# Performance work log

Measured on AMD Instinct MI355X. Metric: run time of the kernel, lower is better.

Reference implementation:

```python
import jax, jax.numpy as jnp
import numpy as np

C = 256        # channels
HEADS = 4
D = C // HEADS # per-head dim
M = 3          # num modalities
EPS = 1e-5
NEG_SLOPE = 0.2  # PyG GATv2 leaky_relu slope


def setup_inputs() -> dict:
    key = jax.random.key(0)
    ks = iter(jax.random.split(key, 40))
    def nrm(shape, s=0.02):
        return jax.random.normal(next(ks), shape, dtype=jnp.float32) * s
    B, H, W = 2, 128, 128
    inp = {}
    for m in range(M):
        inp[f"modal{m}"] = jax.random.normal(next(ks), (B, C, H, W), dtype=jnp.float32)
    # fusion node initializer MLP: Linear-ReLU-Linear
    inp["fn_w1"] = nrm((C, C)); inp["fn_b1"] = jnp.zeros((C,), jnp.float32)
    inp["fn_w2"] = nrm((C, C)); inp["fn_b2"] = jnp.zeros((C,), jnp.float32)
    # two GATv2 layers + layernorms
    for l in range(2):
        inp[f"l{l}_wl"] = nrm((C, C)); inp[f"l{l}_bl"] = jnp.zeros((C,), jnp.float32)
        inp[f"l{l}_wr"] = nrm((C, C)); inp[f"l{l}_br"] = jnp.zeros((C,), jnp.float32)
        inp[f"l{l}_att"] = nrm((HEADS, D), 0.1)
        inp[f"l{l}_bias"] = jnp.zeros((C,), jnp.float32)
        inp[f"ln{l}_g"] = jnp.ones((C,), jnp.float32)
        inp[f"ln{l}_b"] = jnp.zeros((C,), jnp.float32)
    # spatial interaction: conv3x3 (no bias) + BN (eval mode) + ReLU
    inp["conv_w"] = nrm((C, C, 3, 3))
    inp["bn_g"] = jnp.ones((C,), jnp.float32); inp["bn_b"] = jnp.zeros((C,), jnp.float32)
    inp["bn_m"] = jnp.zeros((C,), jnp.float32); inp["bn_v"] = jnp.ones((C,), jnp.float32)
    return inp


def _gatv2(x, wl, bl, wr, br, att, bias):
    # Dense batched GATv2 over P tiny complete graphs (self-loops included,
    # matching PyG GATv2Conv add_self_loops=True default).
    P, N, Cc = x.shape
    xl = (x @ wl + bl).reshape(P, N, HEADS, D)  # source / message features
    xr = (x @ wr + br).reshape(P, N, HEADS, D)  # target features
    e = jax.nn.leaky_relu(xr[:, :, None] + xl[:, None, :], NEG_SLOPE)  # [P,Ni,Nj,H,D]
    scores = jnp.einsum('pijhd,hd->pijh', e, att)
    alpha = jax.nn.softmax(scores, axis=2)  # softmax over source nodes j per target i
    out = jnp.einsum('pijh,pjhd->pihd', alpha, xl)
    return out.reshape(P, N, Cc) + bias


def _layernorm(x, g, b):
    mu = jnp.mean(x, axis=-1, keepdims=True)
    var = jnp.mean((x - mu) ** 2, axis=-1, keepdims=True)
    return (x - mu) * jax.lax.rsqrt(var + EPS) * g + b


def _forward(modal0, modal1, modal2, fn_w1, fn_b1, fn_w2, fn_b2,
             l0_wl, l0_bl, l0_wr, l0_br, l0_att, l0_bias, ln0_g, ln0_b,
             l1_wl, l1_bl, l1_wr, l1_br, l1_att, l1_bias, ln1_g, ln1_b,
             conv_w, bn_g, bn_b, bn_m, bn_v):
    B, _, H, W = modal0.shape
    stacked = jnp.stack([modal0, modal1, modal2], axis=1)        # [B,M,C,H,W]
    modal_nodes = stacked.transpose(0, 3, 4, 1, 2).reshape(-1, M, C)  # [P,M,C]
    mean_feat = jnp.mean(modal_nodes, axis=1, keepdims=True)     # [P,1,C]
    fusion = jax.nn.relu(mean_feat @ fn_w1 + fn_b1) @ fn_w2 + fn_b2
    x = jnp.concatenate([fusion, modal_nodes], axis=1)           # [P,M+1,C]
    for (wl, bl, wr, br, att, bias, g, b) in (
        (l0_wl, l0_bl, l0_wr, l0_br, l0_att, l0_bias, ln0_g, ln0_b),
        (l1_wl, l1_bl, l1_wr, l1_br, l1_att, l1_bias, ln1_g, ln1_b),
    ):
        x = _layernorm(_gatv2(x, wl, bl, wr, br, att, bias) + x, g, b)
    fused = x[:, 0, :].reshape(B, H, W, C).transpose(0, 3, 1, 2)  # [B,C,H,W]
    y = jax.lax.conv_general_dilated(
        fused, conv_w, window_strides=(1, 1), padding='SAME',
        dimension_numbers=('NCHW', 'OIHW', 'NCHW'))
    bc = lambda v: v[None, :, None, None]
    y = (y - bc(bn_m)) * bc(jax.lax.rsqrt(bn_v + EPS)) * bc(bn_g) + bc(bn_b)
    y = jax.nn.relu(y)
    return y + fused


def reference(modal0, modal1, modal2, fn_w1, fn_b1, fn_w2, fn_b2,
              l0_wl, l0_bl, l0_wr, l0_br, l0_att, l0_bias, ln0_g, ln0_b,
              l1_wl, l1_bl, l1_wr, l1_br, l1_att, l1_bias, ln1_g, ln1_b,
              conv_w, bn_g, bn_b, bn_m, bn_v):
    return _forward(modal0, modal1, modal2, fn_w1, fn_b1, fn_w2, fn_b2,
                    l0_wl, l0_bl, l0_wr, l0_br, l0_att, l0_bias, ln0_g, ln0_b,
                    l1_wl, l1_bl, l1_wr, l1_br, l1_att, l1_bias, ln1_g, ln1_b,
                    conv_w, bn_g, bn_b, bn_m, bn_v)
```

## Files before the change

kernel.cpp:

```cpp
#include <hip/hip_runtime.h>


#define Pn 32768
#define PADR 16900

typedef __attribute__((ext_vector_type(8))) short bf16x8;
typedef __attribute__((ext_vector_type(4))) float f32x4;
typedef __attribute__((ext_vector_type(4))) unsigned short u16x4;
typedef __attribute__((ext_vector_type(8))) unsigned short u16x8;
typedef __attribute__((ext_vector_type(2))) unsigned int u32x2;

__device__ __forceinline__ float b2f(short s) {
  unsigned u = ((unsigned)(unsigned short)s) << 16;
  float f;
  __builtin_memcpy(&f, &u, 4);
  return f;
}
__device__ __forceinline__ float asf(unsigned u) {
  float f;
  __builtin_memcpy(&f, &u, 4);
  return f;
}
__device__ __forceinline__ short f2b(float f) {
  unsigned u;
  __builtin_memcpy(&u, &f, 4);
  u += 0x7fffu + ((u >> 16) & 1u);
  return (short)(u >> 16);
}
__device__ __forceinline__ float ldany(const void* p, int i, int bf) {
  return bf ? b2f(((const short*)p)[i]) : ((const float*)p)[i];
}
__device__ __forceinline__ void gload_lds16(const short* g, short* l) {
  __builtin_amdgcn_global_load_lds(
      (const __attribute__((address_space(1))) unsigned int*)g,
      (__attribute__((address_space(3))) unsigned int*)l, 16, 0, 0);
}

template <int CTRL>
__device__ __forceinline__ float dpp_add(float v) {
  int s;
  __builtin_memcpy(&s, &v, 4);
  int m = __builtin_amdgcn_update_dpp(0, s, CTRL, 0xF, 0xF, false);
  float f;
  __builtin_memcpy(&f, &m, 4);
  return v + f;
}
__device__ __forceinline__ float rsum16(float v) {
  v = dpp_add<0x121>(v);
  v = dpp_add<0x122>(v);
  v = dpp_add<0x124>(v);
  v = dpp_add<0x128>(v);
  return v;
}

__global__ __launch_bounds__(256) void detect_dtype(const void* probe, int* flag) {
  const short* s = (const short*)probe;
  int cnt = 0;
#pragma unroll
  for (int i = 0; i < 8; ++i) {
    short v = s[(threadIdx.x * 8 + i) * 2];
    int e = ((unsigned short)v >> 7) & 0xFF;
    cnt += (e >= 100 && e <= 127) ? 1 : 0;
  }
  __shared__ int tot;
  if (threadIdx.x == 0) tot = 0;
  __syncthreads();
  atomicAdd(&tot, cnt);
  __syncthreads();
  if (threadIdx.x == 0) flag[0] = (tot > 1024) ? 1 : 0;
}

struct P18 { const void* p[18]; };
__global__ __launch_bounds__(256) void prep_params(P18 s, const int* flag, float* pb) {
  int bf = *flag;
  int t = threadIdx.x;
#pragma unroll
  for (int v = 0; v < 18; ++v) pb[v * 256 + t] = ldany(s.p[v], t, bf);
}

__global__ __launch_bounds__(256) void prep_gemm_w(
    const void* w0, const void* w1, const void* w2, const void* w3,
    const void* w4, const void* w5, const int* flag, short* wt) {
  int bf = *flag;
  const void* src;
  switch (blockIdx.y) {
    case 0: src = w0; break;
    case 1: src = w1; break;
    case 2: src = w2; break;
    case 3: src = w3; break;
    case 4: src = w4; break;
    default: src = w5; break;
  }
  int idx = blockIdx.x * 256 + threadIdx.x;
  int n = idx >> 8, k = idx & 255;
  wt[blockIdx.y * 65536 + idx] = f2b(ldany(src, k * 256 + n, bf));
}

__global__ __launch_bounds__(256) void prep_conv_w(const void* cw, const int* flag,
                                                   short* cwt) {
  int bf = *flag;
  int idx = blockIdx.x * 256 + threadIdx.x;
  int tap = idx >> 16;
  int n = (idx >> 8) & 255;
  int k = idx & 255;
  cwt[idx] = f2b(ldany(cw, (n * 256 + k) * 9 + tap, bf));
}

__global__ __launch_bounds__(256) void zero_border(short* rowsPad) {
  int id = blockIdx.x;
  int b = id >= 516;
  int r = id - b * 516;
  int hp, wp;
  if (r < 130)      { hp = 0;       wp = r; }
  else if (r < 260) { hp = 129;     wp = r - 130; }
  else if (r < 388) { hp = r - 259; wp = 0; }
  else              { hp = r - 387; wp = 129; }
  rowsPad[(b * PADR + hp * 130 + wp) * 256 + threadIdx.x] = 0;
}

__global__ __launch_bounds__(256) void gather_chunk(
    const void* m0, const void* m1, const void* m2, const int* flag,
    short* Xc, short* meanc, int sb0) {
  const int bf = *flag;
  const int bx = blockIdx.x;
  const int seg = bx >> 2;
  const int cb = (bx & 3) * 64;
  const int sb = sb0 + seg;
  const int wt = sb & 1, h = (sb >> 1) & 127, b = sb >> 8;
  const int w0 = wt * 64;
  const int lp0 = seg * 64;
  const int t = threadIdx.x;

  __shared__ short tile[3][64][72];
  const void* srcs[3] = {m0, m1, m2};

  const int lsub = t & 7;
#pragma unroll
  for (int pass = 0; pass < 2; ++pass) {
    int c_l = pass * 32 + (t >> 3);
    long long gbase = ((long long)(b * 256 + cb + c_l) * 128 + h) * 128 + w0 + lsub * 8;
#pragma unroll
    for (int m = 0; m < 3; ++m) {
      u16x8 v;
      if (bf) {
        v = *(const u16x8*)((const short*)srcs[m] + gbase);
      } else {
        const float* gp = (const float*)srcs[m] + gbase;
        f32x4 f0 = *(const f32x4*)gp;
        f32x4 f1 = *(const f32x4*)(gp + 4);
#pragma unroll
        for (int k = 0; k < 4; ++k) {
          v[k] = (unsigned short)f2b(f0[k]);
          v[4 + k] = (unsigned short)f2b(f1[k]);
        }
      }
      *(u16x8*)&tile[m][c_l][lsub * 8] = v;
    }
  }
  __syncthreads();

  const int c0 = (t & 7) * 8;
#pragma unroll
  for (int pass = 0; pass < 2; ++pass) {
    int w_l = pass * 32 + (t >> 3);
    float mv[8];
#pragma unroll
    for (int m = 0; m < 3; ++m) {
      u16x8 v;
#pragma unroll
      for (int k = 0; k < 8; ++k) {
        short s = tile[m][c0 + k][w_l];
        v[k] = (unsigned short)s;
        float f = b2f(s);
        mv[k] = (m == 0) ? f : mv[k] + f;
      }
      *(u16x8*)(Xc + (long long)((lp0 + w_l) * 4 + 1 + m) * 256 + cb + c0) = v;
    }
    u16x8 mb;
#pragma unroll
    for (int k = 0; k < 8; ++k)
      mb[k] = (unsigned short)f2b(mv[k] * (1.f / 3.f));
    *(u16x8*)(meanc + (long long)(lp0 + w_l) * 256 + cb + c0) = mb;
  }
}

template <int RELU>
__global__ __launch_bounds__(256) void gemm_tile(
    const short* __restrict__ A, const short* __restrict__ Bt,
    const float* __restrict__ bias, short* __restrict__ out, int ostride) {
  __shared__ short lds[2][16384];
  const int t = threadIdx.x;
  const int l = t & 63, wv = t >> 6;
  const int m0 = blockIdx.x * 128;
  const int n0 = blockIdx.y * 128;
  const int r = l & 15, q = l >> 4;
  const int wm = wv & 1, wn = wv >> 1;

  f32x4 acc[4][4];
#pragma unroll
  for (int a = 0; a < 4; ++a)
#pragma unroll
    for (int c = 0; c < 4; ++c) acc[a][c] = (f32x4){0.f, 0.f, 0.f, 0.f};

  auto stage = [&](int kt, int bufi) {
    const int k0 = kt * 64;
#pragma unroll
    for (int j = 0; j < 4; ++j) {
      int flat = (j * 4 + wv) * 64 + l;
      int row = flat >> 3;
      int cs = (flat & 7) ^ (row & 7);
      gload_lds16(A + (m0 + row) * 256 + k0 + cs * 8,
                  &lds[bufi][(j * 4 + wv) * 512]);
      gload_lds16(Bt + (n0 + row) * 256 + k0 + cs * 8,
                  &lds[bufi][8192 + (j * 4 + wv) * 512]);
    }
  };
  auto step = [&](int bufi, int nkt) {
    bf16x8 af[2][4], bfr[2][4];
#pragma unroll
    for (int kh = 0; kh < 2; ++kh) {
#pragma unroll
      for (int a = 0; a < 4; ++a) {
        int R = wm * 64 + a * 16 + r;
        int s = (kh * 4 + q) ^ (R & 7);
        af[kh][a] = *(const bf16x8*)(&lds[bufi][R * 64 + s * 8]);
      }
#pragma unroll
      for (int c = 0; c < 4; ++c) {
        int R = wn * 64 + c * 16 + r;
        int s = (kh * 4 + q) ^ (R & 7);
        bfr[kh][c] = *(const bf16x8*)(&lds[bufi][8192 + R * 64 + s * 8]);
      }
    }
    if (nkt >= 0) stage(nkt, bufi ^ 1);
#pragma unroll
    for (int kh = 0; kh < 2; ++kh)
#pragma unroll
      for (int a = 0; a < 4; ++a)
#pragma unroll
        for (int c = 0; c < 4; ++c)
          acc[a][c] = __builtin_amdgcn_mfma_f32_16x16x32_bf16(
              af[kh][a], bfr[kh][c], acc[a][c], 0, 0, 0);
    if (nkt >= 0) __syncthreads();
  };

  stage(0, 0);
  __syncthreads();
  step(0, 1);
  step(1, 2);
  step(0, 3);
  step(1, -1);

#pragma unroll
  for (int c = 0; c < 4; ++c) {
    int n = n0 + wn * 64 + c * 16 + r;
    float bs = bias[n];
#pragma unroll
    for (int a = 0; a < 4; ++a)
#pragma unroll
      for (int i = 0; i < 4; ++i) {
        int m = m0 + wm * 64 + a * 16 + q * 4 + i;
        float v = acc[a][c][i] + bs;
        if (RELU) v = fmaxf(v, 0.f);
        out[m * ostride + n] = f2b(v);
      }
  }
}

__global__ __launch_bounds__(256) void attn_ln(
    const short* __restrict__ XLRc,
    const float* __restrict__ att, const float* __restrict__ bias,
    const float* __restrict__ lng, const float* __restrict__ lnb,
    short* __restrict__ Xc, int pOff, short* rowsPad, short* fimgb,
    int writeFused) {
  const int lane = threadIdx.x & 63;
  const int wv = threadIdx.x >> 6;
  const int e = lane & 15;
  const int lp = blockIdx.x * 16 + wv * 4 + (lane >> 4);
  const int pg = pOff + lp;

  float out[4][4][4];
#pragma unroll
  for (int h = 0; h < 4; ++h) {
    float av[4];
#pragma unroll
    for (int k = 0; k < 4; ++k) av[k] = att[h * 64 + e * 4 + k];
    float xlf[4][4], xrf[4][4];
#pragma unroll
    for (int j = 0; j < 4; ++j) {
      const short* rb = XLRc + (lp * 4 + j) * 512 + h * 64 + e * 4;
      u32x2 xl2 = *(const u32x2*)rb;
      u32x2 xr2 = *(const u32x2*)(rb + 256);
      xlf[j][0] = asf(xl2[0] << 16); xlf[j][1] = asf(xl2[0] & 0xffff0000u);
      xlf[j][2] = asf(xl2[1] << 16); xlf[j][3] = asf(xl2[1] & 0xffff0000u);
      xrf[j][0] = asf(xr2[0] << 16); xrf[j][1] = asf(xr2[0] & 0xffff0000u);
      xrf[j][2] = asf(xr2[1] << 16); xrf[j][3] = asf(xr2[1] & 0xffff0000u);
    }
    float rp[4], lp_[4];
#pragma unroll
    for (int j = 0; j < 4; ++j) {
      float r = 0.f, l2 = 0.f;
#pragma unroll
      for (int k = 0; k < 4; ++k) {
        r += xrf[j][k] * av[k];
        l2 += xlf[j][k] * av[k];
      }
      rp[j] = r;
      lp_[j] = l2;
    }
#pragma unroll
    for (int i = 0; i < 4; ++i) {
      float s[4];
#pragma unroll
      for (int j = 0; j < 4; ++j) {
        float acc = 0.f;
#pragma unroll
        for (int k = 0; k < 4; ++k) {
          float t = xrf[i][k] + xlf[j][k];
          acc += __builtin_fabsf(t) * av[k];
        }
        float ap = 0.6f * (rp[i] + lp_[j]) + 0.4f * acc;
        s[j] = rsum16(ap);
      }
      float mx = fmaxf(fmaxf(s[0], s[1]), fmaxf(s[2], s[3]));
      float e0 = __expf(s[0] - mx), e1 = __expf(s[1] - mx);
      float e2 = __expf(s[2] - mx), e3 = __expf(s[3] - mx);
      float inv = __builtin_amdgcn_rcpf(e0 + e1 + e2 + e3);
      float a0 = e0 * inv, a1 = e1 * inv, a2 = e2 * inv, a3 = e3 * inv;
#pragma unroll
      for (int k = 0; k < 4; ++k)
        out[i][h][k] =
            a0 * xlf[0][k] + a1 * xlf[1][k] + a2 * xlf[2][k] + a3 * xlf[3][k];
    }
  }

  float biasf[4][4];
#pragma unroll
  for (int h = 0; h < 4; ++h)
#pragma unroll
    for (int k = 0; k < 4; ++k) biasf[h][k] = bias[h * 64 + e * 4 + k];

#pragma unroll
  for (int i = 0; i < 4; ++i) {
    float y[4][4], sm = 0.f;
#pragma unroll
    for (int h = 0; h < 4; ++h) {
      u32x2 rv2 = *(const u32x2*)(Xc + (lp * 4 + i) * 256 + h * 64 + e * 4);
      float r0 = asf(rv2[0] << 16), r1 = asf(rv2[0] & 0xffff0000u);
      float r2 = asf(rv2[1] << 16), r3 = asf(rv2[1] & 0xffff0000u);
      y[h][0] = out[i][h][0] + biasf[h][0] + r0;
      y[h][1] = out[i][h][1] + biasf[h][1] + r1;
      y[h][2] = out[i][h][2] + biasf[h][2] + r2;
      y[h][3] = out[i][h][3] + biasf[h][3] + r3;
      sm += y[h][0] + y[h][1] + y[h][2] + y[h][3];
    }
    sm = rsum16(sm);
    float mu = sm * (1.f / 256.f);
    float vs = 0.f;
#pragma unroll
    for (int h = 0; h < 4; ++h)
#pragma unroll
      for (int k = 0; k < 4; ++k) {
        float d = y[h][k] - mu;
        vs += d * d;
      }
    vs = rsum16(vs);
    float rs = rsqrtf(vs * (1.f / 256.f) + 1e-5f);
#pragma unroll
    for (int h = 0; h < 4; ++h) {
      float g0 = lng[h * 64 + e * 4 + 0], g1 = lng[h * 64 + e * 4 + 1];
      float g2 = lng[h * 64 + e * 4 + 2], g3 = lng[h * 64 + e * 4 + 3];
      float b0 = lnb[h * 64 + e * 4 + 0], b1 = lnb[h * 64 + e * 4 + 1];
      float b2 = lnb[h * 64 + e * 4 + 2], b3 = lnb[h * 64 + e * 4 + 3];
      u16x4 ov;
      ov[0] = (unsigned short)f2b((y[h][0] - mu) * rs * g0 + b0);
      ov[1] = (unsigned short)f2b((y[h][1] - mu) * rs * g1 + b1);
      ov[2] = (unsigned short)f2b((y[h][2] - mu) * rs * g2 + b2);
      ov[3] = (unsigned short)f2b((y[h][3] - mu) * rs * g3 + b3);
      *(u16x4*)(Xc + (lp * 4 + i) * 256 + h * 64 + e * 4) = ov;
      if (writeFused && i == 0) {
        int w = pg & 127, hh = (pg >> 7) & 127, b = pg >> 14;
        *(u16x4*)(rowsPad + (b * PADR + (hh + 1) * 130 + (w + 1)) * 256 +
                  h * 64 + e * 4) = ov;
#pragma unroll
        for (int k = 0; k < 4; ++k) {
          int c = h * 64 + e * 4 + k;
          fimgb[((b * 256 + c) * 128 + hh) * 128 + w] = (short)ov[k];
        }
      }
    }
  }
}

__global__ __launch_bounds__(256) void conv_tile(
    const short* __restrict__ cwt, const short* __restrict__ rowsPad,
    const short* __restrict__ fimgb, const float* __restrict__ bnp,
    const int* __restrict__ flag, void* __restrict__ outp) {
  __shared__ short lds[2][16384];
  const int bf = *flag;
  const int t = threadIdx.x;
  const int l = t & 63, wv = t >> 6;
  const int pb = blockIdx.x;
  const int bb = pb >> 7, h = pb & 127;
  const int m0 = blockIdx.y * 128;
  const int r = l & 15, q = l >> 4;
  const int wm = wv & 1, wn = wv >> 1;

  f32x4 acc[4][4];
#pragma unroll
  for (int a = 0; a < 4; ++a)
#pragma unroll
    for (int c = 0; c < 4; ++c) acc[a][c] = (f32x4){0.f, 0.f, 0.f, 0.f};

  auto stage = [&](int stp, int bufi) {
    const int tap = stp >> 2, kt = stp & 3;
    const int ty = (tap >= 6) ? 2 : (tap >= 3 ? 1 : 0);
    const int tx = tap - ty * 3;
    const int prow0 = bb * PADR + (h + ty) * 130 + tx;
    const short* Abase = cwt + tap * 65536;
    const int k0 = kt * 64;
#pragma unroll
    for (int j = 0; j < 4; ++j) {
      int flat = (j * 4 + wv) * 64 + l;
      int row = flat >> 3;
      int cs = (flat & 7) ^ (row & 7);
      gload_lds16(Abase + (m0 + row) * 256 + k0 + cs * 8,
                  &lds[bufi][(j * 4 + wv) * 512]);
      gload_lds16(rowsPad + (prow0 + row) * 256 + k0 + cs * 8,
                  &lds[bufi][8192 + (j * 4 + wv) * 512]);
    }
  };

  stage(0, 0);
  __syncthreads();
  int cur = 0;
  for (int stp = 0; stp < 36; ++stp) {
    bf16x8 af[2][4], bfr[2][4];
#pragma unroll
    for (int kh = 0; kh < 2; ++kh) {
#pragma unroll
      for (int a = 0; a < 4; ++a) {
        int R = wm * 64 + a * 16 + r;
        int s = (kh * 4 + q) ^ (R & 7);
        af[kh][a] = *(const bf16x8*)(&lds[cur][R * 64 + s * 8]);
      }
#pragma unroll
      for (int c = 0; c < 4; ++c) {
        int R = wn * 64 + c * 16 + r;
        int s = (kh * 4 + q) ^ (R & 7);
        bfr[kh][c] = *(const bf16x8*)(&lds[cur][8192 + R * 64 + s * 8]);
      }
    }
    if (stp < 35) stage(stp + 1, cur ^ 1);
#pragma unroll
    for (int kh = 0; kh < 2; ++kh)
#pragma unroll
      for (int a = 0; a < 4; ++a)
#pragma unroll
        for (int c = 0; c < 4; ++c)
          acc[a][c] = __builtin_amdgcn_mfma_f32_16x16x32_bf16(
              af[kh][a], bfr[kh][c], acc[a][c], 0, 0, 0);
    if (stp < 35) { __syncthreads(); cur ^= 1; }
  }

#pragma unroll
  for (int a = 0; a < 4; ++a)
#pragma unroll
    for (int i = 0; i < 4; ++i) {
      int m = m0 + wm * 64 + a * 16 + q * 4 + i;
      float scale = rsqrtf(bnp[768 + m] + 1e-5f) * bnp[m];
      float bmean = bnp[512 + m], bbeta = bnp[256 + m];
      int ib = ((bb * 256 + m) * 128 + h) * 128;
#pragma unroll
      for (int c = 0; c < 4; ++c) {
        int w = wn * 64 + c * 16 + r;
        float v = (acc[a][c][i] - bmean) * scale + bbeta;
        v = fmaxf(v, 0.f);
        int idx = ib + w;
        float res = v + b2f(fimgb[idx]);
        if (bf) ((short*)outp)[idx] = f2b(res);
        else    ((float*)outp)[idx] = res;
      }
    }
}

extern "C" void kernel_launch(void* const* d_in, const int* in_sizes, int n_in,
                              void* d_out, int out_size, void* d_ws, size_t ws_size,
                              hipStream_t stream) {
  const long long baseS = 18033680LL;
  int NCH = 8;
  for (int cand = 1; cand <= 8; cand <<= 1) {
    long long tot = (baseS + (32768LL / cand) * 3072LL) * 2LL;
    if (tot <= (long long)ws_size) { NCH = cand; break; }
  }
  const int CPIX = 32768 / NCH;

  short* ws = (short*)d_ws;
  short* FROWSP = ws;
  short* FIMG   = ws + 8652800;
  short* WT     = ws + 17041408;
  short* CWT    = ws + 17434624;
  float* PB     = (float*)(ws + 18024448);
  int*   FLAG   = (int*)(ws + 18033664);
  short* XLRc   = ws + 18033680;
  short* Xc     = XLRc + (long long)CPIX * 2048;
  short* MEANc  = XLRc;
  short* H1c    = XLRc + (long long)CPIX * 256;

  detect_dtype<<<1, 256, 0, stream>>>(d_in[3], FLAG);

  P18 pp;
  pp.p[0] = d_in[4];   pp.p[1] = d_in[6];
  pp.p[2] = d_in[8];   pp.p[3] = d_in[10];
  pp.p[4] = d_in[11];  pp.p[5] = d_in[12];
  pp.p[6] = d_in[13];  pp.p[7] = d_in[14];
  pp.p[8] = d_in[16];  pp.p[9] = d_in[18];
  pp.p[10] = d_in[19]; pp.p[11] = d_in[20];
  pp.p[12] = d_in[21]; pp.p[13] = d_in[22];
  pp.p[14] = d_in[24]; pp.p[15] = d_in[25];
  pp.p[16] = d_in[26]; pp.p[17] = d_in[27];
  prep_params<<<1, 256, 0, stream>>>(pp, FLAG, PB);

  prep_gemm_w<<<dim3(256, 6), 256, 0, stream>>>(d_in[3], d_in[5], d_in[7],
                                                d_in[9], d_in[15], d_in[17],
                                                FLAG, WT);
  prep_conv_w<<<2304, 256, 0, stream>>>(d_in[23], FLAG, CWT);
  zero_border<<<1032, 256, 0, stream>>>(FROWSP);

  for (int ci = 0; ci < NCH; ++ci) {
    gather_chunk<<<(CPIX / 64) * 4, 256, 0, stream>>>(d_in[0], d_in[1], d_in[2],
                                                      FLAG, Xc, MEANc,
                                                      ci * (CPIX / 64));
    gemm_tile<1><<<dim3(CPIX / 128, 2), 256, 0, stream>>>(
        MEANc, WT + 0 * 65536, PB + 0 * 256, H1c, 256);
    gemm_tile<0><<<dim3(CPIX / 128, 2), 256, 0, stream>>>(
        H1c, WT + 1 * 65536, PB + 1 * 256, Xc, 1024);
    for (int lyr = 0; lyr < 2; ++lyr) {
      gemm_tile<0><<<dim3(4 * CPIX / 128, 4), 256, 0, stream>>>(
          Xc, WT + (2 + 2 * lyr) * 65536, PB + (2 + 6 * lyr) * 256, XLRc, 512);
      attn_ln<<<CPIX / 16, 256, 0, stream>>>(
          XLRc, PB + (4 + 6 * lyr) * 256, PB + (5 + 6 * lyr) * 256,
          PB + (6 + 6 * lyr) * 256, PB + (7 + 6 * lyr) * 256, Xc, ci * CPIX,
          FROWSP, FIMG, lyr);
    }
  }

  conv_tile<<<dim3(256, 2), 256, 0, stream>>>(CWT, FROWSP, FIMG, PB + 14 * 256,
                                              FLAG, d_out);
}
```

Baseline: 607.3 us.

## Pre-swizzle weights into MFMA fragment order and load B directly from global

Weights are repacked at prep time into the per-lane MFMA fragment layout, so the GEMM reads B fragments straight from global/L2 instead of staging them through LDS. Only the activation tile A goes through LDS, with a smaller 32-wide K step and an XOR swizzle, which shrinks LDS use and allows three blocks per CU via launch bounds. The grid is reordered so blocks sharing an M tile launch next to each other, improving A reuse in cache. The cost is more global-load latency on B per K step, which is not hidden by a double buffer, and more synchronisation steps.

```diff
diff --git a/kernel.cpp b/kernel.cpp
--- a/kernel.cpp
+++ b/kernel.cpp
@@ -92,7 +92,13 @@
     default: src = w5; break;
   }
   int idx = blockIdx.x * 256 + threadIdx.x;
-  int n = idx >> 8, k = idx & 255;
+  int ntile = idx >> 12;
+  int kt = (idx >> 9) & 7;
+  int l = (idx >> 3) & 63;
+  int j = idx & 7;
+  int r = l & 15, q = l >> 4;
+  int n = ntile * 16 + r;
+  int k = kt * 32 + q * 8 + j;
   wt[blockIdx.y * 65536 + idx] = f2b(ldany(src, k * 256 + n, bf));
 }
 
@@ -185,17 +191,19 @@
 }
 
 template <int RELU>
-__global__ __launch_bounds__(256) void gemm_tile(
-    const short* __restrict__ A, const short* __restrict__ Bt,
+__global__ __launch_bounds__(256, 3) void gemm_tile(
+    const short* __restrict__ A, const short* __restrict__ Bf,
     const float* __restrict__ bias, short* __restrict__ out, int ostride) {
-  __shared__ short lds[2][16384];
+  __shared__ short lds[2][4096];
   const int t = threadIdx.x;
   const int l = t & 63, wv = t >> 6;
-  const int m0 = blockIdx.x * 128;
-  const int n0 = blockIdx.y * 128;
+  const int n0 = blockIdx.x * 128;
+  const int m0 = blockIdx.y * 128;
   const int r = l & 15, q = l >> 4;
   const int wm = wv & 1, wn = wv >> 1;
 
+  const short* Bw = Bf + (((n0 >> 4) + wn * 4) << 12) + l * 8;
+
   f32x4 acc[4][4];
 #pragma unroll
   for (int a = 0; a < 4; ++a)
@@ -203,53 +211,40 @@
     for (int c = 0; c < 4; ++c) acc[a][c] = (f32x4){0.f, 0.f, 0.f, 0.f};
 
   auto stage = [&](int kt, int bufi) {
-    const int k0 = kt * 64;
-#pragma unroll
-    for (int j = 0; j < 4; ++j) {
-      int flat = (j * 4 + wv) * 64 + l;
-      int row = flat >> 3;
-      int cs = (flat & 7) ^ (row & 7);
-      gload_lds16(A + (m0 + row) * 256 + k0 + cs * 8,
-                  &lds[bufi][(j * 4 + wv) * 512]);
-      gload_lds16(Bt + (n0 + row) * 256 + k0 + cs * 8,
-                  &lds[bufi][8192 + (j * 4 + wv) * 512]);
-    }
-  };
-  auto step = [&](int bufi, int nkt) {
-    bf16x8 af[2][4], bfr[2][4];
-#pragma unroll
-    for (int kh = 0; kh < 2; ++kh) {
-#pragma unroll
-      for (int a = 0; a < 4; ++a) {
-        int R = wm * 64 + a * 16 + r;
-        int s = (kh * 4 + q) ^ (R & 7);
-        af[kh][a] = *(const bf16x8*)(&lds[bufi][R * 64 + s * 8]);
-      }
-#pragma unroll
-      for (int c = 0; c < 4; ++c) {
-        int R = wn * 64 + c * 16 + r;
-        int s = (kh * 4 + q) ^ (R & 7);
-        bfr[kh][c] = *(const bf16x8*)(&lds[bufi][8192 + R * 64 + s * 8]);
-      }
-    }
-    if (nkt >= 0) stage(nkt, bufi ^ 1);
-#pragma unroll
-    for (int kh = 0; kh < 2; ++kh)
-#pragma unroll
-      for (int a = 0; a < 4; ++a)
-#pragma unroll
-        for (int c = 0; c < 4; ++c)
-          acc[a][c] = __builtin_amdgcn_mfma_f32_16x16x32_bf16(
-              af[kh][a], bfr[kh][c], acc[a][c], 0, 0, 0);
-    if (nkt >= 0) __syncthreads();
+    const int k0 = kt * 32;
+#pragma unroll
+    for (int j = 0; j < 2; ++j) {
+      int s0 = j * 256 + wv * 64;
+      int row = (s0 + l) >> 2;
+      int chs = (l & 3) ^ ((row >> 1) & 3);
+      gload_lds16(A + (m0 + row) * 256 + k0 + chs * 8, &lds[bufi][s0 * 8]);
+    }
   };
 
   stage(0, 0);
   __syncthreads();
-  step(0, 1);
-  step(1, 2);
-  step(0, 3);
-  step(1, -1);
+#pragma unroll
+  for (int kt = 0; kt < 8; ++kt) {
+    const int cur = kt & 1;
+    bf16x8 bfr[4], af[4];
+#pragma unroll
+    for (int c = 0; c < 4; ++c)
+      bfr[c] = *(const bf16x8*)(Bw + (c * 8 + kt) * 512);
+#pragma unroll
+    for (int a = 0; a < 4; ++a) {
+      int R = wm * 64 + a * 16 + r;
+      int ch = q ^ ((R >> 1) & 3);
+      af[a] = *(const bf16x8*)(&lds[cur][R * 32 + ch * 8]);
+    }
+    if (kt < 7) stage(kt + 1, cur ^ 1);
+#pragma unroll
+    for (int a = 0; a < 4; ++a)
+#pragma unroll
+      for (int c = 0; c < 4; ++c)
+        acc[a][c] = __builtin_amdgcn_mfma_f32_16x16x32_bf16(
+            af[a], bfr[c], acc[a][c], 0, 0, 0);
+    if (kt < 7) __syncthreads();
+  }
 
 #pragma unroll
   for (int c = 0; c < 4; ++c) {
@@ -531,12 +526,12 @@
     gather_chunk<<<(CPIX / 64) * 4, 256, 0, stream>>>(d_in[0], d_in[1], d_in[2],
                                                       FLAG, Xc, MEANc,
                                                       ci * (CPIX / 64));
-    gemm_tile<1><<<dim3(CPIX / 128, 2), 256, 0, stream>>>(
+    gemm_tile<1><<<dim3(2, CPIX / 128), 256, 0, stream>>>(
         MEANc, WT + 0 * 65536, PB + 0 * 256, H1c, 256);
-    gemm_tile<0><<<dim3(CPIX / 128, 2), 256, 0, stream>>>(
+    gemm_tile<0><<<dim3(2, CPIX / 128), 256, 0, stream>>>(
         H1c, WT + 1 * 65536, PB + 1 * 256, Xc, 1024);
     for (int lyr = 0; lyr < 2; ++lyr) {
-      gemm_tile<0><<<dim3(4 * CPIX / 128, 4), 256, 0, stream>>>(
+      gemm_tile<0><<<dim3(4, 4 * CPIX / 128), 256, 0, stream>>>(
           Xc, WT + (2 + 2 * lyr) * 65536, PB + (2 + 6 * lyr) * 256, XLRc, 512);
       attn_ln<<<CPIX / 16, 256, 0, stream>>>(
           XLRc, PB + (4 + 6 * lyr) * 256, PB + (5 + 6 * lyr) * 256,
```

Measured after the change: 613.0 us. No clear change (+0.9%).
